# Optimization experiments

Measured on AMD Instinct MI355X. Metric: run time of the kernel, lower is better.

## Reference

```python
import jax, jax.numpy as jnp
import numpy as np

BS, C_IN, CTX, TGT = 2, 8, 1024, 96
D_MODEL, N_HEADS, D_FF, N_LAYERS = 256, 16, 1024, 4
PF, SF, PC, SC = 8, 4, 32, 16
NF = (CTX + SF - PF) // SF + 1   # 256 fine patches (incl. end-pad)
NC = (CTX + SC - PC) // SC + 1   # 64 coarse patches
TOTAL = NF + NC                  # 320
EPS = 1e-5
DK = D_MODEL // N_HEADS
SCALE = DK ** -0.5


def _patchify(z, plen, stride):
    # ReplicationPad1d((0, stride)) then unfold -> (bs, c, n_patches, plen)
    pad = jnp.broadcast_to(z[..., -1:], z.shape[:-1] + (stride,))
    zp = jnp.concatenate([z, pad], axis=-1)
    n = (zp.shape[-1] - plen) // stride + 1
    idx = np.arange(n)[:, None] * stride + np.arange(plen)[None, :]
    return zp[..., idx]


def _layernorm(x, s, b):
    m = x.mean(-1, keepdims=True)
    v = jnp.var(x, axis=-1, keepdims=True)
    return (x - m) * jax.lax.rsqrt(v + EPS) * s + b


def setup_inputs() -> dict:
    key = jax.random.key(0)
    ks = jax.random.split(key, 16)
    g = lambda k, shape: jax.random.normal(k, shape, jnp.float32) * 0.02
    return {
        "z": jax.random.normal(ks[0], (BS, C_IN, CTX), jnp.float32),
        "revin_w": jnp.ones((C_IN,), jnp.float32),
        "revin_b": jnp.zeros((C_IN,), jnp.float32),
        "Wf": g(ks[1], (PF, D_MODEL)), "bf": jnp.zeros((D_MODEL,), jnp.float32),
        "Wc": g(ks[2], (PC, D_MODEL)), "bc": jnp.zeros((D_MODEL,), jnp.float32),
        "W_pos": jax.random.uniform(ks[3], (TOTAL, D_MODEL), jnp.float32, -0.02, 0.02),
        "WQ": g(ks[4], (N_LAYERS, D_MODEL, D_MODEL)), "bQ": jnp.zeros((N_LAYERS, D_MODEL), jnp.float32),
        "WK": g(ks[5], (N_LAYERS, D_MODEL, D_MODEL)), "bK": jnp.zeros((N_LAYERS, D_MODEL), jnp.float32),
        "WV": g(ks[6], (N_LAYERS, D_MODEL, D_MODEL)), "bV": jnp.zeros((N_LAYERS, D_MODEL), jnp.float32),
        "WO": g(ks[7], (N_LAYERS, D_MODEL, D_MODEL)), "bO": jnp.zeros((N_LAYERS, D_MODEL), jnp.float32),
        "ln1_s": jnp.ones((N_LAYERS, D_MODEL), jnp.float32), "ln1_b": jnp.zeros((N_LAYERS, D_MODEL), jnp.float32),
        "ln2_s": jnp.ones((N_LAYERS, D_MODEL), jnp.float32), "ln2_b": jnp.zeros((N_LAYERS, D_MODEL), jnp.float32),
        "F1": g(ks[8], (N_LAYERS, D_MODEL, D_FF)), "c1": jnp.zeros((N_LAYERS, D_FF), jnp.float32),
        "F2": g(ks[9], (N_LAYERS, D_FF, D_MODEL)), "c2": jnp.zeros((N_LAYERS, D_MODEL), jnp.float32),
        "Wh": g(ks[10], (D_MODEL * TOTAL, TGT)), "bh": jnp.zeros((TGT,), jnp.float32),
    }


def reference(z, revin_w, revin_b, Wf, bf, Wc, bc, W_pos, WQ, bQ, WK, bK, WV, bV,
              WO, bO, ln1_s, ln1_b, ln2_s, ln2_b, F1, c1, F2, c2, Wh, bh):
    # RevIN norm over the time axis (last axis of (bs, c, T))
    mean = z.mean(-1, keepdims=True)
    std = jnp.sqrt(jnp.var(z, axis=-1, keepdims=True) + EPS)
    zn = (z - mean) / std * revin_w[None, :, None] + revin_b[None, :, None]

    # dual-scale patch embedding
    x_fine = _patchify(zn, PF, SF) @ Wf + bf      # (bs, c, NF, d)
    x_coarse = _patchify(zn, PC, SC) @ Wc + bc    # (bs, c, NC, d)
    x = jnp.concatenate([x_fine, x_coarse], axis=2)  # (bs, c, TOTAL, d)

    u = x.reshape(BS * C_IN, TOTAL, D_MODEL) + W_pos  # (B, S, d), B=bs*c

    # residual-score transformer encoder (post-norm)
    prev = None
    for l in range(N_LAYERS):
        q = (u @ WQ[l] + bQ[l]).reshape(-1, TOTAL, N_HEADS, DK).transpose(0, 2, 1, 3)
        k = (u @ WK[l] + bK[l]).reshape(-1, TOTAL, N_HEADS, DK).transpose(0, 2, 1, 3)
        v = (u @ WV[l] + bV[l]).reshape(-1, TOTAL, N_HEADS, DK).transpose(0, 2, 1, 3)
        s = jnp.einsum('bhqd,bhkd->bhqk', q, k) * SCALE
        if prev is not None:
            s = s + prev
        w = jax.nn.softmax(s, axis=-1)
        o = jnp.einsum('bhqk,bhkd->bhqd', w, v).transpose(0, 2, 1, 3).reshape(-1, TOTAL, D_MODEL)
        o = o @ WO[l] + bO[l]
        u = _layernorm(u + o, ln1_s[l], ln1_b[l])
        h = jax.nn.gelu(u @ F1[l] + c1[l], approximate=False) @ F2[l] + c2[l]
        u = _layernorm(u + h, ln2_s[l], ln2_b[l])
        prev = s

    # head: (bs, c, TOTAL, d) -> permute -> flatten(d, TOTAL) -> linear
    zz = u.reshape(BS, C_IN, TOTAL, D_MODEL).transpose(0, 1, 3, 2).reshape(BS, C_IN, D_MODEL * TOTAL)
    out = zz @ Wh + bh  # (bs, c, TGT)

    # RevIN denorm
    out = (out - revin_b[None, :, None]) / (revin_w[None, :, None] + EPS * EPS) * std + mean
    return out
```

## Files before the change

kernel.cpp:

```cpp
#include <hip/hip_runtime.h>
#include <math.h>

typedef unsigned short ushort;
typedef unsigned int uint;
typedef __attribute__((ext_vector_type(8))) short short8;
typedef __attribute__((ext_vector_type(4))) float f32x4;
typedef __attribute__((ext_vector_type(4))) ushort us4;

constexpr int BS = 2, C_IN = 8, CTX = 1024, TGT = 96;
constexpr int DM = 256, NH = 16, DFF = 1024, NL = 4;
constexpr int NF = 256, TOTAL = 320;
constexpr int NB = 16;
constexpr int DK = 16;
constexpr float EPS = 1e-5f;
constexpr float SCALE = 0.25f;
constexpr int KHEAD = DM * TOTAL;
constexpr int M = NB * TOTAL;

__device__ __forceinline__ ushort f2b(float x) {
    uint u = __float_as_uint(x);
    u += 0x7fff + ((u >> 16) & 1);
    return (ushort)(u >> 16);
}
__device__ __forceinline__ float bu2f(ushort x) { return __uint_as_float(((uint)x) << 16); }
__device__ __forceinline__ float lo2f(uint p) { return __uint_as_float(p << 16); }
__device__ __forceinline__ float hi2f(uint p) { return __uint_as_float(p & 0xffff0000u); }
__device__ __forceinline__ uint pack2(float a, float b) { return (uint)f2b(a) | ((uint)f2b(b) << 16); }

typedef __attribute__((address_space(3))) uint lds_u32;
typedef const __attribute__((address_space(1))) uint glb_u32;
__device__ __forceinline__ void ldst16(const void* g, void* l) {
    __builtin_amdgcn_global_load_lds((glb_u32*)g, (lds_u32*)l, 16, 0, 0);
}

__global__ void k_prep(const float* __restrict__ WQ, const float* __restrict__ WK,
                       const float* __restrict__ WV, const float* __restrict__ WO,
                       const float* __restrict__ F1, const float* __restrict__ F2,
                       const float* __restrict__ Wh,
                       ushort* __restrict__ Wtqkv, ushort* __restrict__ WtO,
                       ushort* __restrict__ Ft1, ushort* __restrict__ Ft2,
                       ushort* __restrict__ WhT2,
                       const float* __restrict__ z, const float* __restrict__ rw,
                       const float* __restrict__ rb, float* __restrict__ zn,
                       float* __restrict__ meanv, float* __restrict__ stdv) {
    __shared__ ushort tile[32][33];
    __shared__ float rr1[16], rr2[16], bcast[2];
    int i = blockIdx.x;
    int tx = threadIdx.x, ty = threadIdx.y;
    if (i < 1024) {
        int zz = i >> 6, w = zz >> 2, l = zz & 3;
        const float* src = (w == 0 ? WQ : (w == 1 ? WK : (w == 2 ? WV : WO))) + l * 65536;
        ushort* dst = (w < 3) ? (Wtqkv + (size_t)l * 768 * 256 + w * 256 * 256)
                              : (WtO + (size_t)l * 65536);
        int c0 = (i & 7) * 32, r0 = ((i >> 3) & 7) * 32;
        tile[ty][tx] = f2b(src[(r0 + ty) * 256 + c0 + tx]);
        __syncthreads();
        dst[(c0 + ty) * 256 + r0 + tx] = tile[tx][ty];
    } else if (i < 2048) {
        int j = i - 1024, l = j >> 8;
        const float* src = F1 + (size_t)l * 262144;
        ushort* dst = Ft1 + (size_t)l * 262144;
        int c0 = (j & 31) * 32, r0 = ((j >> 5) & 7) * 32;
        tile[ty][tx] = f2b(src[(r0 + ty) * 1024 + c0 + tx]);
        __syncthreads();
        dst[(c0 + ty) * 256 + r0 + tx] = tile[tx][ty];
    } else if (i < 3072) {
        int j = i - 2048, l = j >> 8;
        const float* src = F2 + (size_t)l * 262144;
        ushort* dst = Ft2 + (size_t)l * 262144;
        int c0 = (j & 7) * 32, r0 = ((j >> 3) & 31) * 32;
        tile[ty][tx] = f2b(src[(r0 + ty) * 256 + c0 + tx]);
        __syncthreads();
        dst[(c0 + ty) * 1024 + r0 + tx] = tile[tx][ty];
    } else if (i < 10752) {
        int j = i - 3072;
        int t0 = (j % 3) * 32, rest = j / 3;
        int d0 = (rest & 7) * 32, pp = rest >> 3;
        tile[ty][tx] = f2b(Wh[((size_t)(d0 + ty) * 320 + pp) * 96 + t0 + tx]);
        __syncthreads();
        WhT2[(size_t)(t0 + ty) * KHEAD + pp * 256 + d0 + tx] = tile[tx][ty];
    } else {
        int bc = i - 10752;
        int tid = ty * 32 + tx;
        float x = z[bc * CTX + tid];
        float s1 = x, s2 = x * x;
#pragma unroll
        for (int off = 1; off < 64; off <<= 1) {
            s1 += __shfl_xor(s1, off);
            s2 += __shfl_xor(s2, off);
        }
        if ((tid & 63) == 0) { rr1[tid >> 6] = s1; rr2[tid >> 6] = s2; }
        __syncthreads();
        if (tid == 0) {
            float a1 = 0.f, a2 = 0.f;
            for (int k = 0; k < 16; k++) { a1 += rr1[k]; a2 += rr2[k]; }
            float m = a1 * (1.0f / CTX);
            float var = a2 * (1.0f / CTX) - m * m;
            float sd = sqrtf(var + EPS);
            meanv[bc] = m; stdv[bc] = sd;
            bcast[0] = m; bcast[1] = sd;
        }
        __syncthreads();
        float m = bcast[0], sd = bcast[1];
        float w = rw[bc % C_IN], b = rb[bc % C_IN];
        zn[bc * CTX + tid] = (x - m) / sd * w + b;
    }
}

__global__ void k_embed(const float* __restrict__ zn, const float* __restrict__ Wf,
                        const float* __restrict__ bfv, const float* __restrict__ Wc,
                        const float* __restrict__ bcv, const float* __restrict__ Wpos,
                        ushort* __restrict__ u) {
    int bc = blockIdx.x / TOTAL, p = blockIdx.x % TOTAL, d = threadIdx.x;
    float acc;
    if (p < NF) {
        acc = bfv[d];
        int base = p * 4;
        for (int i = 0; i < 8; i++) {
            int idx = min(base + i, CTX - 1);
            acc += zn[bc * CTX + idx] * Wf[i * DM + d];
        }
    } else {
        int pc = p - NF;
        acc = bcv[d];
        int base = pc * 16;
        for (int i = 0; i < 32; i++) {
            int idx = min(base + i, CTX - 1);
            acc += zn[bc * CTX + idx] * Wc[i * DM + d];
        }
    }
    acc += Wpos[p * DM + d];
    u[(bc * TOTAL + p) * DM + d] = f2b(acc);
}

template <int GELU, int QKV>
__global__ __launch_bounds__(256) void k_gemm_mfma(const ushort* __restrict__ A,
                                                   const ushort* __restrict__ Wt,
                                                   const float* __restrict__ b0,
                                                   const float* __restrict__ b1,
                                                   const float* __restrict__ b2,
                                                   ushort* __restrict__ C,
                                                   int Mm, int N, int K) {
    __shared__ ushort As[64][32];
    __shared__ ushort Bs[64][32];
    int tid = threadIdx.x;
    int wave = tid >> 6, lane = tid & 63;
    int quad = lane >> 4, l16 = lane & 15;
    int m0 = blockIdx.y * 64, n0 = blockIdx.x * 64;

    f32x4 acc[4];
#pragma unroll
    for (int nt = 0; nt < 4; nt++) acc[nt] = (f32x4){0.f, 0.f, 0.f, 0.f};

    int srow = wave * 16 + (lane >> 2);
    int sc = (lane & 3) ^ ((srow >> 1) & 3);
    ushort* AsW = &As[wave * 16][0];
    ushort* BsW = &Bs[wave * 16][0];
    const ushort* Ag = &A[(size_t)(m0 + srow) * K + sc * 8];
    const ushort* Bg = &Wt[(size_t)(n0 + srow) * K + sc * 8];
    int rchunk = (quad ^ ((l16 >> 1) & 3)) * 8;

    for (int k0 = 0; k0 < K; k0 += 32) {
        ldst16(Ag + k0, AsW);
        ldst16(Bg + k0, BsW);
        __syncthreads();
        short8 af = *(const short8*)&As[wave * 16 + l16][rchunk];
#pragma unroll
        for (int nt = 0; nt < 4; nt++) {
            short8 bf = *(const short8*)&Bs[nt * 16 + l16][rchunk];
            acc[nt] = __builtin_amdgcn_mfma_f32_16x16x32_bf16(af, bf, acc[nt], 0, 0, 0);
        }
        __syncthreads();
    }
#pragma unroll
    for (int nt = 0; nt < 4; nt++) {
        int col = n0 + nt * 16 + l16;
        float bi;
        if (QKV) {
            int bs = (n0 + nt * 16) >> 8;
            const float* bp = bs == 0 ? b0 : (bs == 1 ? b1 : b2);
            bi = bp[col & 255];
        } else {
            bi = b0[col];
        }
#pragma unroll
        for (int r = 0; r < 4; r++) {
            int rowm = m0 + wave * 16 + quad * 4 + r;
            float vv = acc[nt][r] + bi;
            if (GELU) vv = vv * 0.5f * (1.0f + erff(vv * 0.70710678118f));
            if (QKV) C[(col >> 8) * (M * DM) + rowm * DM + (col & 255)] = f2b(vv);
            else C[rowm * N + col] = f2b(vv);
        }
    }
}

__global__ __launch_bounds__(256) void k_gemm_ln16(const ushort* __restrict__ A,
                                                   const ushort* __restrict__ Wt,
                                                   const float* __restrict__ bias,
                                                   const float* __restrict__ ls,
                                                   const float* __restrict__ lb,
                                                   ushort* __restrict__ u, int K) {
    __shared__ ushort As[16][32];
    __shared__ ushort Bs[256][32];
    __shared__ float ps1[16][4], ps2[16][4];
    int tid = threadIdx.x;
    int wave = tid >> 6, lane = tid & 63;
    int quad = lane >> 4, l16 = lane & 15;
    int m0 = blockIdx.x * 16;

    f32x4 acc[4];
#pragma unroll
    for (int nt = 0; nt < 4; nt++) acc[nt] = (f32x4){0.f, 0.f, 0.f, 0.f};

    int brow = wave * 16 + (lane >> 2);
    int bc_swz = (lane & 3) ^ ((brow >> 1) & 3);
    const ushort* Bg0 = &Wt[(size_t)brow * K + bc_swz * 8];
    ushort* BsW0 = &Bs[wave * 16][0];
    int ar = lane >> 2;
    int ac = (lane & 3) ^ ((ar >> 1) & 3);
    const ushort* Ag = &A[(size_t)(m0 + ar) * K + ac * 8];
    int rchunk = (quad ^ ((l16 >> 1) & 3)) * 8;

    for (int k0 = 0; k0 < K; k0 += 32) {
        if (tid < 64) ldst16(Ag + k0, &As[0][0]);
#pragma unroll
        for (int i = 0; i < 4; i++)
            ldst16(Bg0 + (size_t)i * 64 * K + k0, BsW0 + i * 64 * 32);
        __syncthreads();
        short8 af = *(const short8*)&As[l16][rchunk];
#pragma unroll
        for (int nt = 0; nt < 4; nt++) {
            short8 bf = *(const short8*)&Bs[wave * 64 + nt * 16 + l16][rchunk];
            acc[nt] = __builtin_amdgcn_mfma_f32_16x16x32_bf16(af, bf, acc[nt], 0, 0, 0);
        }
        __syncthreads();
    }
    float xv[4][4];
#pragma unroll
    for (int r = 0; r < 4; r++) {
        int rowg = m0 + quad * 4 + r;
        float s1 = 0.f, s2 = 0.f;
#pragma unroll
        for (int nt = 0; nt < 4; nt++) {
            int col = wave * 64 + nt * 16 + l16;
            float x = acc[nt][r] + bias[col] + bu2f(u[rowg * DM + col]);
            xv[r][nt] = x; s1 += x; s2 += x * x;
        }
        s1 += __shfl_xor(s1, 1); s2 += __shfl_xor(s2, 1);
        s1 += __shfl_xor(s1, 2); s2 += __shfl_xor(s2, 2);
        s1 += __shfl_xor(s1, 4); s2 += __shfl_xor(s2, 4);
        s1 += __shfl_xor(s1, 8); s2 += __shfl_xor(s2, 8);
        if (l16 == 0) { ps1[quad * 4 + r][wave] = s1; ps2[quad * 4 + r][wave] = s2; }
    }
    __syncthreads();
#pragma unroll
    for (int r = 0; r < 4; r++) {
        int rowl = quad * 4 + r, rowg = m0 + rowl;
        float s1 = ps1[rowl][0] + ps1[rowl][1] + ps1[rowl][2] + ps1[rowl][3];
        float s2 = ps2[rowl][0] + ps2[rowl][1] + ps2[rowl][2] + ps2[rowl][3];
        float m = s1 * (1.0f / DM);
        float var = s2 * (1.0f / DM) - m * m;
        float rs = rsqrtf(var + EPS);
#pragma unroll
        for (int nt = 0; nt < 4; nt++) {
            int col = wave * 64 + nt * 16 + l16;
            u[rowg * DM + col] = f2b((xv[r][nt] - m) * rs * ls[col] + lb[col]);
        }
    }
}

template <int MODE>
__global__ __launch_bounds__(256, 4) void k_attn(const ushort* __restrict__ qm, const ushort* __restrict__ km,
                                                 const ushort* __restrict__ vm, uint4* __restrict__ sp,
                                                 ushort* __restrict__ ao) {
    __shared__ ushort sh[10240];
    uint* sh32 = (uint*)sh;
    int bh = blockIdx.x, b = bh >> 4, h = bh & 15;
    int i0 = blockIdx.y * 64;
    int t = threadIdx.x, wave = t >> 6, lane = t & 63, quad = lane >> 4, l16 = lane & 15;
    const short8 zero8 = (short8){0, 0, 0, 0, 0, 0, 0, 0};

    int cb = (bh * 5 + (int)blockIdx.y) * 10 * 256 + t;
    uint4 pv[10];
    if (MODE) {
#pragma unroll
        for (int c = 0; c < 10; c++) pv[c] = sp[cb + c * 256];
    }

    for (int idx = t; idx < 640; idx += 256) {
        int j = idx >> 1, half = idx & 1;
        short8 kv = *(const short8*)&km[(b * TOTAL + j) * DM + h * DK + half * 8];
        int jt = j >> 4, jl = j & 15;
        *(short8*)&sh[((jt * 2 + half) * 16 + jl) * 8] = kv;
    }
    for (int idx = t; idx < 320; idx += 256) {
        int jp = idx >> 1, dh = idx & 1;
        int j = jp * 2;
        uint4 a = *(const uint4*)&vm[(b * TOTAL + j) * DM + h * DK + dh * 8];
        uint4 bb = *(const uint4*)&vm[(b * TOTAL + j + 1) * DM + h * DK + dh * 8];
        const ushort* ap = (const ushort*)&a;
        const ushort* bp = (const ushort*)&bb;
        int jr = j & 31;
        int q = (jr & 15) >> 2, jj = ((jr >> 4) << 2) + (jr & 3);
        int base = 5120 + ((j >> 5) * 4 + q) * 128 + jj;
#pragma unroll
        for (int dd = 0; dd < 8; dd++) {
            int d = dh * 8 + dd;
            uint val = (uint)ap[dd] | ((uint)bp[dd] << 16);
            sh32[(base + d * 8) >> 1] = val;
        }
    }
    short8 qf = zero8;
    if (quad < 2) qf = *(const short8*)&qm[(b * TOTAL + i0 + wave * 16 + l16) * DM + h * DK + quad * 8];
    __syncthreads();

    f32x4 acc[20];
    if (MODE) {
#pragma unroll
        for (int c = 0; c < 10; c++) {
            acc[2 * c][0] = lo2f(pv[c].x) * 4.0f;
            acc[2 * c][1] = hi2f(pv[c].x) * 4.0f;
            acc[2 * c][2] = lo2f(pv[c].y) * 4.0f;
            acc[2 * c][3] = hi2f(pv[c].y) * 4.0f;
            acc[2 * c + 1][0] = lo2f(pv[c].z) * 4.0f;
            acc[2 * c + 1][1] = hi2f(pv[c].z) * 4.0f;
            acc[2 * c + 1][2] = lo2f(pv[c].w) * 4.0f;
            acc[2 * c + 1][3] = hi2f(pv[c].w) * 4.0f;
        }
    } else {
#pragma unroll
        for (int nt = 0; nt < 20; nt++) acc[nt] = (f32x4){0.f, 0.f, 0.f, 0.f};
    }
#pragma unroll
    for (int nt = 0; nt < 20; nt++) {
        short8 kf = *(const short8*)&sh[((nt * 2 + (quad & 1)) * 16 + l16) * 8];
        acc[nt] = __builtin_amdgcn_mfma_f32_16x16x32_bf16(kf, qf, acc[nt], 0, 0, 0);
    }

#pragma unroll
    for (int c = 0; c < 10; c++) {
        float e[8];
#pragma unroll
        for (int j = 0; j < 8; j++) e[j] = acc[2 * c + (j >> 2)][j & 3] * SCALE;
        if (MODE != 2) {
            uint4 ov;
            ov.x = pack2(e[0], e[1]); ov.y = pack2(e[2], e[3]);
            ov.z = pack2(e[4], e[5]); ov.w = pack2(e[6], e[7]);
            sp[cb + c * 256] = ov;
        }
#pragma unroll
        for (int j = 0; j < 8; j++) acc[2 * c + (j >> 2)][j & 3] = e[j];
    }

    float mx = -1e30f;
#pragma unroll
    for (int nt = 0; nt < 20; nt++)
#pragma unroll
        for (int r = 0; r < 4; r++) mx = fmaxf(mx, acc[nt][r]);
    mx = fmaxf(mx, __shfl_xor(mx, 16));
    mx = fmaxf(mx, __shfl_xor(mx, 32));
    float sum = 0.f;
#pragma unroll
    for (int nt = 0; nt < 20; nt++)
#pragma unroll
        for (int r = 0; r < 4; r++) { acc[nt][r] = __expf(acc[nt][r] - mx); sum += acc[nt][r]; }
    sum += __shfl_xor(sum, 16);
    sum += __shfl_xor(sum, 32);
    float inv = 1.f / sum;
#pragma unroll
    for (int nt = 0; nt < 20; nt++)
#pragma unroll
        for (int r = 0; r < 4; r++) acc[nt][r] *= inv;

    f32x4 oacc = (f32x4){0.f, 0.f, 0.f, 0.f};
#pragma unroll
    for (int jt2 = 0; jt2 < 10; jt2++) {
        short8 vt = *(const short8*)&sh[5120 + ((jt2 * 4 + quad) * 16 + l16) * 8];
        union { short8 v; uint u[4]; } pf;
        pf.u[0] = pack2(acc[2 * jt2][0], acc[2 * jt2][1]);
        pf.u[1] = pack2(acc[2 * jt2][2], acc[2 * jt2][3]);
        pf.u[2] = pack2(acc[2 * jt2 + 1][0], acc[2 * jt2 + 1][1]);
        pf.u[3] = pack2(acc[2 * jt2 + 1][2], acc[2 * jt2 + 1][3]);
        oacc = __builtin_amdgcn_mfma_f32_16x16x32_bf16(vt, pf.v, oacc, 0, 0, 0);
    }
    us4 ov4 = (us4){f2b(oacc[0]), f2b(oacc[1]), f2b(oacc[2]), f2b(oacc[3])};
    *(us4*)&ao[(b * TOTAL + i0 + wave * 16 + l16) * DM + h * DK + quad * 4] = ov4;
}

__global__ __launch_bounds__(256) void k_head(const ushort* __restrict__ u, const ushort* __restrict__ WhT2,
                                              float* __restrict__ part) {
    int t0 = blockIdx.x * 16;
    int wave = threadIdx.x >> 6, lane = threadIdx.x & 63;
    int quad = lane >> 4, l16 = lane & 15;
    int chunk = blockIdx.y * 4 + wave;
    int kbeg = chunk * 1024;
    f32x4 acc = (f32x4){0.f, 0.f, 0.f, 0.f};
    const ushort* za = &u[(size_t)l16 * KHEAD + quad * 8];
    const ushort* wb = &WhT2[(size_t)(t0 + l16) * KHEAD + quad * 8];
#pragma unroll 4
    for (int k = kbeg; k < kbeg + 1024; k += 32) {
        short8 af = *(const short8*)&za[k];
        short8 bf = *(const short8*)&wb[k];
        acc = __builtin_amdgcn_mfma_f32_16x16x32_bf16(af, bf, acc, 0, 0, 0);
    }
#pragma unroll
    for (int r = 0; r < 4; r++)
        part[(size_t)chunk * (NB * TGT) + (quad * 4 + r) * TGT + t0 + l16] = acc[r];
}

__global__ void k_final(const float* __restrict__ part, const float* __restrict__ bh,
                        const float* __restrict__ rw, const float* __restrict__ rb,
                        const float* __restrict__ meanv, const float* __restrict__ stdv,
                        float* __restrict__ out) {
    int idx = blockIdx.x * 256 + threadIdx.x;
    if (idx >= NB * TGT) return;
    int bc = idx / TGT, t = idx % TGT, c = bc % C_IN;
    float vv = bh[t];
#pragma unroll 8
    for (int j = 0; j < 80; j++) vv += part[(size_t)j * (NB * TGT) + idx];
    vv = (vv - rb[c]) / (rw[c] + EPS * EPS) * stdv[bc] + meanv[bc];
    out[idx] = vv;
}

extern "C" void kernel_launch(void* const* d_in, const int* in_sizes, int n_in,
                              void* d_out, int out_size, void* d_ws, size_t ws_size,
                              hipStream_t stream) {
    const float* z       = (const float*)d_in[0];
    const float* revin_w = (const float*)d_in[1];
    const float* revin_b = (const float*)d_in[2];
    const float* Wf      = (const float*)d_in[3];
    const float* bfv     = (const float*)d_in[4];
    const float* Wc      = (const float*)d_in[5];
    const float* bcv     = (const float*)d_in[6];
    const float* Wpos    = (const float*)d_in[7];
    const float* WQ      = (const float*)d_in[8];
    const float* bQ      = (const float*)d_in[9];
    const float* WK      = (const float*)d_in[10];
    const float* bK      = (const float*)d_in[11];
    const float* WV      = (const float*)d_in[12];
    const float* bV      = (const float*)d_in[13];
    const float* WO      = (const float*)d_in[14];
    const float* bO      = (const float*)d_in[15];
    const float* ln1s    = (const float*)d_in[16];
    const float* ln1b    = (const float*)d_in[17];
    const float* ln2s    = (const float*)d_in[18];
    const float* ln2b    = (const float*)d_in[19];
    const float* F1      = (const float*)d_in[20];
    const float* c1      = (const float*)d_in[21];
    const float* F2      = (const float*)d_in[22];
    const float* c2      = (const float*)d_in[23];
    const float* Wh      = (const float*)d_in[24];
    const float* bh      = (const float*)d_in[25];
    float* out = (float*)d_out;

    char* p = (char*)d_ws;
    float* meanv = (float*)p;    p += 16 * 4;
    float* stdv  = (float*)p;    p += 16 * 4;
    p = (char*)(((size_t)p + 255) & ~255ull);
    float* part = (float*)p;     p += (size_t)80 * NB * TGT * 4;
    float* zn = (float*)p;       p += NB * CTX * 4;
    ushort* u    = (ushort*)p;   p += (size_t)M * DM * 2;
    ushort* qkv  = (ushort*)p;   p += (size_t)3 * M * DM * 2;
    ushort* ax   = (ushort*)p;   p += (size_t)M * DM * 2;
    ushort* hbuf = (ushort*)p;   p += (size_t)M * DFF * 2;
    ushort* Wtqkv = (ushort*)p;  p += (size_t)NL * 768 * 256 * 2;
    ushort* WtO   = (ushort*)p;  p += (size_t)NL * 256 * 256 * 2;
    ushort* Ft1   = (ushort*)p;  p += (size_t)NL * 1024 * 256 * 2;
    ushort* Ft2   = (ushort*)p;  p += (size_t)NL * 256 * 1024 * 2;
    ushort* WhT2  = (ushort*)p;  p += (size_t)TGT * KHEAD * 2;
    p = (char*)(((size_t)p + 255) & ~255ull);
    uint4* sp = (uint4*)p;       p += (size_t)NB * NH * 5 * 10 * 256 * 16;

    k_prep<<<10768, dim3(32, 32), 0, stream>>>(WQ, WK, WV, WO, F1, F2, Wh,
                                               Wtqkv, WtO, Ft1, Ft2, WhT2,
                                               z, revin_w, revin_b, zn, meanv, stdv);
    k_embed<<<NB * TOTAL, 256, 0, stream>>>(zn, Wf, bfv, Wc, bcv, Wpos, u);

    for (int l = 0; l < NL; l++) {
        k_gemm_mfma<0, 1><<<dim3(12, 80), 256, 0, stream>>>(
            u, Wtqkv + (size_t)l * 768 * 256, bQ + l * DM, bK + l * DM, bV + l * DM, qkv, M, 768, 256);
        if (l == 0)
            k_attn<0><<<dim3(NB * NH, 5), 256, 0, stream>>>(qkv, qkv + M * DM, qkv + 2 * M * DM, sp, ax);
        else if (l == NL - 1)
            k_attn<2><<<dim3(NB * NH, 5), 256, 0, stream>>>(qkv, qkv + M * DM, qkv + 2 * M * DM, sp, ax);
        else
            k_attn<1><<<dim3(NB * NH, 5), 256, 0, stream>>>(qkv, qkv + M * DM, qkv + 2 * M * DM, sp, ax);
        k_gemm_ln16<<<M / 16, 256, 0, stream>>>(
            ax, WtO + (size_t)l * 65536, bO + l * DM, ln1s + l * DM, ln1b + l * DM, u, 256);
        k_gemm_mfma<1, 0><<<dim3(16, 80), 256, 0, stream>>>(
            u, Ft1 + (size_t)l * 262144, c1 + l * DFF, c1, c1, hbuf, M, 1024, 256);
        k_gemm_ln16<<<M / 16, 256, 0, stream>>>(
            hbuf, Ft2 + (size_t)l * 262144, c2 + l * DM, ln2s + l * DM, ln2b + l * DM, u, 1024);
    }

    k_head<<<dim3(TGT / 16, 20), 256, 0, stream>>>(u, WhT2, part);
    k_final<<<(NB * TGT + 255) / 256, 256, 0, stream>>>(part, bh, revin_w, revin_b, meanv, stdv, out);
}
```

Measured before the change: 481.7 us.

## Fuse embed into prep, recompute residual scores from stored Q/K, fold head finalize

The patch embedding is folded into the RevIN branch of the prep kernel, which drops the separate embed launch and the zn buffer. Attention no longer stores and reloads the bf16 residual score matrix. It keeps Q and K for every layer and re-accumulates QK^T over all previous layers in fp32, which adds MMA work and K loads per layer but removes large score traffic and a rounding step. The head kernel now atomically adds scaled partials straight into an output pre-initialized with bias and denorm terms, so k_final and the partial buffer go away. Since the embed work now runs inside only 16 prep blocks, the embedding stage gets much less parallelism.

```diff
diff --git a/kernel.cpp b/kernel.cpp
--- a/kernel.cpp
+++ b/kernel.cpp
@@ -23,8 +23,6 @@
     return (ushort)(u >> 16);
 }
 __device__ __forceinline__ float bu2f(ushort x) { return __uint_as_float(((uint)x) << 16); }
-__device__ __forceinline__ float lo2f(uint p) { return __uint_as_float(p << 16); }
-__device__ __forceinline__ float hi2f(uint p) { return __uint_as_float(p & 0xffff0000u); }
 __device__ __forceinline__ uint pack2(float a, float b) { return (uint)f2b(a) | ((uint)f2b(b) << 16); }
 
 typedef __attribute__((address_space(3))) uint lds_u32;
@@ -41,10 +39,15 @@
                        ushort* __restrict__ Ft1, ushort* __restrict__ Ft2,
                        ushort* __restrict__ WhT2,
                        const float* __restrict__ z, const float* __restrict__ rw,
-                       const float* __restrict__ rb, float* __restrict__ zn,
-                       float* __restrict__ meanv, float* __restrict__ stdv) {
+                       const float* __restrict__ rb,
+                       const float* __restrict__ Wf, const float* __restrict__ bfv,
+                       const float* __restrict__ Wc, const float* __restrict__ bcv,
+                       const float* __restrict__ Wpos, ushort* __restrict__ u,
+                       const float* __restrict__ bhv, float* __restrict__ outp,
+                       float* __restrict__ scalef) {
     __shared__ ushort tile[32][33];
     __shared__ float rr1[16], rr2[16], bcast[2];
+    __shared__ float szn[1024];
     int i = blockIdx.x;
     int tx = threadIdx.x, ty = threadIdx.y;
     if (i < 1024) {
@@ -97,40 +100,36 @@
             float m = a1 * (1.0f / CTX);
             float var = a2 * (1.0f / CTX) - m * m;
             float sd = sqrtf(var + EPS);
-            meanv[bc] = m; stdv[bc] = sd;
             bcast[0] = m; bcast[1] = sd;
         }
         __syncthreads();
         float m = bcast[0], sd = bcast[1];
-        float w = rw[bc % C_IN], b = rb[bc % C_IN];
-        zn[bc * CTX + tid] = (x - m) / sd * w + b;
-    }
-}
-
-__global__ void k_embed(const float* __restrict__ zn, const float* __restrict__ Wf,
-                        const float* __restrict__ bfv, const float* __restrict__ Wc,
-                        const float* __restrict__ bcv, const float* __restrict__ Wpos,
-                        ushort* __restrict__ u) {
-    int bc = blockIdx.x / TOTAL, p = blockIdx.x % TOTAL, d = threadIdx.x;
-    float acc;
-    if (p < NF) {
-        acc = bfv[d];
-        int base = p * 4;
-        for (int i = 0; i < 8; i++) {
-            int idx = min(base + i, CTX - 1);
-            acc += zn[bc * CTX + idx] * Wf[i * DM + d];
-        }
-    } else {
-        int pc = p - NF;
-        acc = bcv[d];
-        int base = pc * 16;
-        for (int i = 0; i < 32; i++) {
-            int idx = min(base + i, CTX - 1);
-            acc += zn[bc * CTX + idx] * Wc[i * DM + d];
-        }
-    }
-    acc += Wpos[p * DM + d];
-    u[(bc * TOTAL + p) * DM + d] = f2b(acc);
+        int c = bc & 7;
+        float w = rw[c], bb = rb[c];
+        szn[tid] = (x - m) / sd * w + bb;
+        if (tid < TGT) outp[bc * TGT + tid] = (bhv[tid] - bb) / (w + EPS * EPS) * sd + m;
+        if (tid == 0) scalef[bc] = sd / (w + EPS * EPS);
+        __syncthreads();
+        for (int o = tid; o < TOTAL * DM; o += 1024) {
+            int p = o >> 8, d = o & 255;
+            float acc2;
+            if (p < NF) {
+                acc2 = bfv[d];
+                int base = p * 4;
+#pragma unroll
+                for (int q = 0; q < 8; q++)
+                    acc2 += szn[min(base + q, CTX - 1)] * Wf[q * DM + d];
+            } else {
+                acc2 = bcv[d];
+                int base = (p - NF) * 16;
+#pragma unroll
+                for (int q = 0; q < 32; q++)
+                    acc2 += szn[min(base + q, CTX - 1)] * Wc[q * DM + d];
+            }
+            acc2 += Wpos[p * DM + d];
+            u[((size_t)bc * TOTAL + p) * DM + d] = f2b(acc2);
+        }
+    }
 }
 
 template <int GELU, int QKV>
@@ -140,6 +139,7 @@
                                                    const float* __restrict__ b1,
                                                    const float* __restrict__ b2,
                                                    ushort* __restrict__ C,
+                                                   ushort* __restrict__ C2,
                                                    int Mm, int N, int K) {
     __shared__ ushort As[64][32];
     __shared__ ushort Bs[64][32];
@@ -188,8 +188,14 @@
             int rowm = m0 + wave * 16 + quad * 4 + r;
             float vv = acc[nt][r] + bi;
             if (GELU) vv = vv * 0.5f * (1.0f + erff(vv * 0.70710678118f));
-            if (QKV) C[(col >> 8) * (M * DM) + rowm * DM + (col & 255)] = f2b(vv);
-            else C[rowm * N + col] = f2b(vv);
+            if (QKV) {
+                int bs = col >> 8;
+                ushort* dst = (bs == 2) ? (C2 + (size_t)rowm * DM)
+                                        : (C + (size_t)bs * (M * DM) + (size_t)rowm * DM);
+                dst[col & 255] = f2b(vv);
+            } else {
+                C[(size_t)rowm * N + col] = f2b(vv);
+            }
         }
     }
 }
@@ -243,7 +249,7 @@
 #pragma unroll
         for (int nt = 0; nt < 4; nt++) {
             int col = wave * 64 + nt * 16 + l16;
-            float x = acc[nt][r] + bias[col] + bu2f(u[rowg * DM + col]);
+            float x = acc[nt][r] + bias[col] + bu2f(u[(size_t)rowg * DM + col]);
             xv[r][nt] = x; s1 += x; s2 += x * x;
         }
         s1 += __shfl_xor(s1, 1); s2 += __shfl_xor(s2, 1);
@@ -264,15 +270,13 @@
 #pragma unroll
         for (int nt = 0; nt < 4; nt++) {
             int col = wave * 64 + nt * 16 + l16;
-            u[rowg * DM + col] = f2b((xv[r][nt] - m) * rs * ls[col] + lb[col]);
-        }
-    }
-}
-
-template <int MODE>
-__global__ __launch_bounds__(256, 4) void k_attn(const ushort* __restrict__ qm, const ushort* __restrict__ km,
-                                                 const ushort* __restrict__ vm, uint4* __restrict__ sp,
-                                                 ushort* __restrict__ ao) {
+            u[(size_t)rowg * DM + col] = f2b((xv[r][nt] - m) * rs * ls[col] + lb[col]);
+        }
+    }
+}
+
+__global__ __launch_bounds__(256, 4) void k_attn(const ushort* __restrict__ qk, const ushort* __restrict__ vm,
+                                                 ushort* __restrict__ ao, int nj) {
     __shared__ ushort sh[10240];
     uint* sh32 = (uint*)sh;
     int bh = blockIdx.x, b = bh >> 4, h = bh & 15;
@@ -280,24 +284,15 @@
     int t = threadIdx.x, wave = t >> 6, lane = t & 63, quad = lane >> 4, l16 = lane & 15;
     const short8 zero8 = (short8){0, 0, 0, 0, 0, 0, 0, 0};
 
-    int cb = (bh * 5 + (int)blockIdx.y) * 10 * 256 + t;
-    uint4 pv[10];
-    if (MODE) {
-#pragma unroll
-        for (int c = 0; c < 10; c++) pv[c] = sp[cb + c * 256];
-    }
-
-    for (int idx = t; idx < 640; idx += 256) {
-        int j = idx >> 1, half = idx & 1;
-        short8 kv = *(const short8*)&km[(b * TOTAL + j) * DM + h * DK + half * 8];
-        int jt = j >> 4, jl = j & 15;
-        *(short8*)&sh[((jt * 2 + half) * 16 + jl) * 8] = kv;
-    }
+    f32x4 acc[20];
+#pragma unroll
+    for (int nt = 0; nt < 20; nt++) acc[nt] = (f32x4){0.f, 0.f, 0.f, 0.f};
+
     for (int idx = t; idx < 320; idx += 256) {
         int jp = idx >> 1, dh = idx & 1;
         int j = jp * 2;
-        uint4 a = *(const uint4*)&vm[(b * TOTAL + j) * DM + h * DK + dh * 8];
-        uint4 bb = *(const uint4*)&vm[(b * TOTAL + j + 1) * DM + h * DK + dh * 8];
+        uint4 a = *(const uint4*)&vm[((size_t)b * TOTAL + j) * DM + h * DK + dh * 8];
+        uint4 bb = *(const uint4*)&vm[((size_t)b * TOTAL + j + 1) * DM + h * DK + dh * 8];
         const ushort* ap = (const ushort*)&a;
         const ushort* bp = (const ushort*)&bb;
         int jr = j & 31;
@@ -310,53 +305,32 @@
             sh32[(base + d * 8) >> 1] = val;
         }
     }
-    short8 qf = zero8;
-    if (quad < 2) qf = *(const short8*)&qm[(b * TOTAL + i0 + wave * 16 + l16) * DM + h * DK + quad * 8];
-    __syncthreads();
-
-    f32x4 acc[20];
-    if (MODE) {
-#pragma unroll
-        for (int c = 0; c < 10; c++) {
-            acc[2 * c][0] = lo2f(pv[c].x) * 4.0f;
-            acc[2 * c][1] = hi2f(pv[c].x) * 4.0f;
-            acc[2 * c][2] = lo2f(pv[c].y) * 4.0f;
-            acc[2 * c][3] = hi2f(pv[c].y) * 4.0f;
-            acc[2 * c + 1][0] = lo2f(pv[c].z) * 4.0f;
-            acc[2 * c + 1][1] = hi2f(pv[c].z) * 4.0f;
-            acc[2 * c + 1][2] = lo2f(pv[c].w) * 4.0f;
-            acc[2 * c + 1][3] = hi2f(pv[c].w) * 4.0f;
-        }
-    } else {
-#pragma unroll
-        for (int nt = 0; nt < 20; nt++) acc[nt] = (f32x4){0.f, 0.f, 0.f, 0.f};
-    }
-#pragma unroll
-    for (int nt = 0; nt < 20; nt++) {
-        short8 kf = *(const short8*)&sh[((nt * 2 + (quad & 1)) * 16 + l16) * 8];
-        acc[nt] = __builtin_amdgcn_mfma_f32_16x16x32_bf16(kf, qf, acc[nt], 0, 0, 0);
-    }
-
-#pragma unroll
-    for (int c = 0; c < 10; c++) {
-        float e[8];
-#pragma unroll
-        for (int j = 0; j < 8; j++) e[j] = acc[2 * c + (j >> 2)][j & 3] * SCALE;
-        if (MODE != 2) {
-            uint4 ov;
-            ov.x = pack2(e[0], e[1]); ov.y = pack2(e[2], e[3]);
-            ov.z = pack2(e[4], e[5]); ov.w = pack2(e[6], e[7]);
-            sp[cb + c * 256] = ov;
-        }
-#pragma unroll
-        for (int j = 0; j < 8; j++) acc[2 * c + (j >> 2)][j & 3] = e[j];
+
+    for (int jl = 0; jl < nj; jl++) {
+        const ushort* qm = qk + (size_t)(2 * jl) * M * DM;
+        const ushort* km = qm + (size_t)M * DM;
+        for (int idx = t; idx < 640; idx += 256) {
+            int j = idx >> 1, half = idx & 1;
+            short8 kv = *(const short8*)&km[((size_t)b * TOTAL + j) * DM + h * DK + half * 8];
+            int jt = j >> 4, jln = j & 15;
+            *(short8*)&sh[((jt * 2 + half) * 16 + jln) * 8] = kv;
+        }
+        short8 qf = zero8;
+        if (quad < 2) qf = *(const short8*)&qm[((size_t)b * TOTAL + i0 + wave * 16 + l16) * DM + h * DK + quad * 8];
+        __syncthreads();
+#pragma unroll
+        for (int nt = 0; nt < 20; nt++) {
+            short8 kf = *(const short8*)&sh[((nt * 2 + (quad & 1)) * 16 + l16) * 8];
+            acc[nt] = __builtin_amdgcn_mfma_f32_16x16x32_bf16(kf, qf, acc[nt], 0, 0, 0);
+        }
+        __syncthreads();
     }
 
     float mx = -1e30f;
 #pragma unroll
     for (int nt = 0; nt < 20; nt++)
 #pragma unroll
-        for (int r = 0; r < 4; r++) mx = fmaxf(mx, acc[nt][r]);
+        for (int r = 0; r < 4; r++) { acc[nt][r] *= SCALE; mx = fmaxf(mx, acc[nt][r]); }
     mx = fmaxf(mx, __shfl_xor(mx, 16));
     mx = fmaxf(mx, __shfl_xor(mx, 32));
     float sum = 0.f;
@@ -384,11 +358,11 @@
         oacc = __builtin_amdgcn_mfma_f32_16x16x32_bf16(vt, pf.v, oacc, 0, 0, 0);
     }
     us4 ov4 = (us4){f2b(oacc[0]), f2b(oacc[1]), f2b(oacc[2]), f2b(oacc[3])};
-    *(us4*)&ao[(b * TOTAL + i0 + wave * 16 + l16) * DM + h * DK + quad * 4] = ov4;
+    *(us4*)&ao[((size_t)b * TOTAL + i0 + wave * 16 + l16) * DM + h * DK + quad * 4] = ov4;
 }
 
 __global__ __launch_bounds__(256) void k_head(const ushort* __restrict__ u, const ushort* __restrict__ WhT2,
-                                              float* __restrict__ part) {
+                                              const float* __restrict__ scalef, float* __restrict__ out) {
     int t0 = blockIdx.x * 16;
     int wave = threadIdx.x >> 6, lane = threadIdx.x & 63;
     int quad = lane >> 4, l16 = lane & 15;
@@ -404,22 +378,10 @@
         acc = __builtin_amdgcn_mfma_f32_16x16x32_bf16(af, bf, acc, 0, 0, 0);
     }
 #pragma unroll
-    for (int r = 0; r < 4; r++)
-        part[(size_t)chunk * (NB * TGT) + (quad * 4 + r) * TGT + t0 + l16] = acc[r];
-}
-
-__global__ void k_final(const float* __restrict__ part, const float* __restrict__ bh,
-                        const float* __restrict__ rw, const float* __restrict__ rb,
-                        const float* __restrict__ meanv, const float* __restrict__ stdv,
-                        float* __restrict__ out) {
-    int idx = blockIdx.x * 256 + threadIdx.x;
-    if (idx >= NB * TGT) return;
-    int bc = idx / TGT, t = idx % TGT, c = bc % C_IN;
-    float vv = bh[t];
-#pragma unroll 8
-    for (int j = 0; j < 80; j++) vv += part[(size_t)j * (NB * TGT) + idx];
-    vv = (vv - rb[c]) / (rw[c] + EPS * EPS) * stdv[bc] + meanv[bc];
-    out[idx] = vv;
+    for (int r = 0; r < 4; r++) {
+        int bcr = quad * 4 + r;
+        atomicAdd(&out[bcr * TGT + t0 + l16], acc[r] * scalef[bcr]);
+    }
 }
 
 extern "C" void kernel_launch(void* const* d_in, const int* in_sizes, int n_in,
@@ -454,45 +416,37 @@
     float* out = (float*)d_out;
 
     char* p = (char*)d_ws;
-    float* meanv = (float*)p;    p += 16 * 4;
-    float* stdv  = (float*)p;    p += 16 * 4;
+    float* scalef = (float*)p;   p += 16 * 4;
     p = (char*)(((size_t)p + 255) & ~255ull);
-    float* part = (float*)p;     p += (size_t)80 * NB * TGT * 4;
-    float* zn = (float*)p;       p += NB * CTX * 4;
-    ushort* u    = (ushort*)p;   p += (size_t)M * DM * 2;
-    ushort* qkv  = (ushort*)p;   p += (size_t)3 * M * DM * 2;
-    ushort* ax   = (ushort*)p;   p += (size_t)M * DM * 2;
-    ushort* hbuf = (ushort*)p;   p += (size_t)M * DFF * 2;
+    ushort* u     = (ushort*)p;  p += (size_t)M * DM * 2;
+    ushort* qkbuf = (ushort*)p;  p += (size_t)NL * 2 * M * DM * 2;
+    ushort* vbuf  = (ushort*)p;  p += (size_t)M * DM * 2;
+    ushort* ax    = (ushort*)p;  p += (size_t)M * DM * 2;
+    ushort* hbuf  = (ushort*)p;  p += (size_t)M * DFF * 2;
     ushort* Wtqkv = (ushort*)p;  p += (size_t)NL * 768 * 256 * 2;
     ushort* WtO   = (ushort*)p;  p += (size_t)NL * 256 * 256 * 2;
     ushort* Ft1   = (ushort*)p;  p += (size_t)NL * 1024 * 256 * 2;
     ushort* Ft2   = (ushort*)p;  p += (size_t)NL * 256 * 1024 * 2;
     ushort* WhT2  = (ushort*)p;  p += (size_t)TGT * KHEAD * 2;
-    p = (char*)(((size_t)p + 255) & ~255ull);
-    uint4* sp = (uint4*)p;       p += (size_t)NB * NH * 5 * 10 * 256 * 16;
 
     k_prep<<<10768, dim3(32, 32), 0, stream>>>(WQ, WK, WV, WO, F1, F2, Wh,
                                                Wtqkv, WtO, Ft1, Ft2, WhT2,
-                                               z, revin_w, revin_b, zn, meanv, stdv);
-    k_embed<<<NB * TOTAL, 256, 0, stream>>>(zn, Wf, bfv, Wc, bcv, Wpos, u);
+                                               z, revin_w, revin_b,
+                                               Wf, bfv, Wc, bcv, Wpos, u,
+                                               bh, out, scalef);
 
     for (int l = 0; l < NL; l++) {
         k_gemm_mfma<0, 1><<<dim3(12, 80), 256, 0, stream>>>(
-            u, Wtqkv + (size_t)l * 768 * 256, bQ + l * DM, bK + l * DM, bV + l * DM, qkv, M, 768, 256);
-        if (l == 0)
-            k_attn<0><<<dim3(NB * NH, 5), 256, 0, stream>>>(qkv, qkv + M * DM, qkv + 2 * M * DM, sp, ax);
-        else if (l == NL - 1)
-            k_attn<2><<<dim3(NB * NH, 5), 256, 0, stream>>>(qkv, qkv + M * DM, qkv + 2 * M * DM, sp, ax);
-        else
-            k_attn<1><<<dim3(NB * NH, 5), 256, 0, stream>>>(qkv, qkv + M * DM, qkv + 2 * M * DM, sp, ax);
+            u, Wtqkv + (size_t)l * 768 * 256, bQ + l * DM, bK + l * DM, bV + l * DM,
+            qkbuf + (size_t)l * 2 * M * DM, vbuf, M, 768, 256);
+        k_attn<<<dim3(NB * NH, 5), 256, 0, stream>>>(qkbuf, vbuf, ax, l + 1);
         k_gemm_ln16<<<M / 16, 256, 0, stream>>>(
             ax, WtO + (size_t)l * 65536, bO + l * DM, ln1s + l * DM, ln1b + l * DM, u, 256);
         k_gemm_mfma<1, 0><<<dim3(16, 80), 256, 0, stream>>>(
-            u, Ft1 + (size_t)l * 262144, c1 + l * DFF, c1, c1, hbuf, M, 1024, 256);
+            u, Ft1 + (size_t)l * 262144, c1 + l * DFF, c1, c1, hbuf, hbuf, M, 1024, 256);
         k_gemm_ln16<<<M / 16, 256, 0, stream>>>(
             hbuf, Ft2 + (size_t)l * 262144, c2 + l * DM, ln2s + l * DM, ln2b + l * DM, u, 1024);
     }
 
-    k_head<<<dim3(TGT / 16, 20), 256, 0, stream>>>(u, WhT2, part);
-    k_final<<<(NB * TGT + 255) / 256, 256, 0, stream>>>(part, bh, revin_w, revin_b, meanv, stdv, out);
-}
+    k_head<<<dim3(TGT / 16, 20), 256, 0, stream>>>(u, WhT2, scalef, out);
+}
```

Result: slower. 536.1 us (+11.3%).
